# Optimization experiments

Hardware: AMD Instinct MI355X
Metric: run time of the kernel (lower is better)

Reference implementation:

```python
import jax, jax.numpy as jnp
import numpy as np

B, T_CTX, N_EMBD, N_ATTN, N_HEAD = 8, 1024, 1024, 1024, 16
HEAD_SIZE = N_ATTN // N_HEAD


def _init_time_w():
    # replicates the torch init: per-head exponential decay curves
    curve = np.array([-(T_CTX - 1 - i) for i in range(T_CTX)], dtype=np.float64)
    ww = np.ones((N_HEAD, T_CTX), dtype=np.float32)
    for h in range(N_HEAD):
        if h < N_HEAD - 1:
            decay_speed = T_CTX ** (-(h + 1) / (N_HEAD - 1))
        else:
            decay_speed = 0.0
        ww[h] = np.exp(curve * decay_speed).astype(np.float32)
    return jnp.asarray(ww)


def setup_inputs() -> dict:
    key = jax.random.key(0)
    ks = jax.random.split(key, 6)
    s = 0.02
    return {
        "x": jax.random.normal(ks[0], (B, T_CTX, N_EMBD), jnp.float32),
        "time_w": _init_time_w(),                                   # [H, TT]
        "time_alpha": jnp.ones((N_HEAD, 1, T_CTX), jnp.float32),
        "time_beta": jnp.ones((N_HEAD, T_CTX, 1), jnp.float32),
        "time_gamma": jnp.ones((T_CTX, 1), jnp.float32),
        "Wk": jax.random.normal(ks[1], (N_ATTN, N_EMBD), jnp.float32) * s,
        "bk": jnp.zeros((N_ATTN,), jnp.float32),
        "Wv": jax.random.normal(ks[2], (N_ATTN, N_EMBD), jnp.float32) * s,
        "bv": jnp.zeros((N_ATTN,), jnp.float32),
        "Wr": jax.random.normal(ks[3], (N_ATTN, N_EMBD), jnp.float32) * s,
        "br": jnp.zeros((N_ATTN,), jnp.float32),
        "Wo": jax.random.normal(ks[4], (N_EMBD, N_ATTN), jnp.float32) * s,
        "bo": jnp.zeros((N_EMBD,), jnp.float32),
    }


def _build_w(time_w, time_alpha, time_beta, T):
    # w[h,t,u] = time_w[h, TT-1-(t-u)] for u<=t else 0  (causal decay matrix)
    TT = time_w.shape[1]
    t = jnp.arange(T)[:, None]
    u = jnp.arange(T)[None, :]
    idx = jnp.clip((TT - 1) - t + u, 0, TT - 1)
    mask = u <= t
    w = jnp.where(mask[None, :, :], time_w[:, idx], 0.0)  # [H, T, T]
    return w * time_alpha[:, :, :T] * time_beta[:, :T, :]


def reference(x, time_w, time_alpha, time_beta, time_gamma,
              Wk, bk, Wv, bv, Wr, br, Wo, bo):
    Bb, T, C = x.shape
    H = time_w.shape[0]
    w = _build_w(time_w, time_alpha, time_beta, T)  # [H,T,T]

    # time shift on the first half of channels: prepend zero row, drop last
    x_half = jnp.pad(x[:, :, : C // 2], ((0, 0), (1, 0), (0, 0)))[:, :T, :]
    xs = jnp.concatenate([x_half, x[:, :, C // 2 :]], axis=-1)

    k = xs @ Wk.T + bk
    v = xs @ Wv.T + bv
    r = xs @ Wr.T + br

    k = jnp.exp(jnp.clip(k, -60.0, 30.0))
    sum_k = jnp.cumsum(k, axis=1)  # [B,T,NA]

    kv = (k * v).reshape(Bb, T, H, -1)               # [B,T,H,hs]
    wkv = jnp.einsum('htu,buhc->bthc', w, kv).reshape(Bb, T, -1)

    rwkv = jax.nn.sigmoid(r) * wkv / sum_k
    out = rwkv @ Wo.T + bo
    return out * time_gamma[:T]
```

## Files before the change

kernel.cpp:

```cpp
#include <hip/hip_runtime.h>
#include <hip/hip_bf16.h>
#include <cstddef>
#include <cstdint>

#define B_SZ   8
#define T_CTX  1024
#define C_DIM  1024
#define H_NUM  16
#define HS     64
#define M_ROWS (B_SZ * T_CTX)

typedef __attribute__((ext_vector_type(8))) short bf16x8;
typedef __attribute__((ext_vector_type(8))) unsigned short u16x8;
typedef __attribute__((ext_vector_type(4))) float f32x4;

static __device__ inline unsigned short f2bf(float f) {
    __hip_bfloat16 h = __float2bfloat16(f);
    return __builtin_bit_cast(unsigned short, h);
}
static __device__ inline float bf2f(unsigned short u) {
    unsigned int v = ((unsigned int)u) << 16;
    return __builtin_bit_cast(float, v);
}
static __device__ inline void gld16(const void* g, void* l) {
    __builtin_amdgcn_global_load_lds((const __attribute__((address_space(1))) void*)g,
                                     (__attribute__((address_space(3))) void*)l,
                                     16, 0, 0);
}

__global__ __launch_bounds__(256)
void convert_all(const float* __restrict__ x, unsigned short* __restrict__ xs,
                 const float* __restrict__ Wk, const float* __restrict__ Wv,
                 const float* __restrict__ Wr, const float* __restrict__ Wo,
                 unsigned short* __restrict__ wdst)
{
    const int bid = blockIdx.x;
    if (bid < 8192) {
        const int idx = (bid * 256 + threadIdx.x) * 4;
        const int m = idx >> 10;
        const int c = idx & 1023;
        float4 v;
        if (c < 512) {
            const int t = m & (T_CTX - 1);
            if (t == 0) v = make_float4(0.f, 0.f, 0.f, 0.f);
            else        v = *(const float4*)(x + (size_t)(m - 1) * C_DIM + c);
        } else {
            v = *(const float4*)(x + idx);
        }
        ushort4 o;
        o.x = f2bf(v.x); o.y = f2bf(v.y); o.z = f2bf(v.z); o.w = f2bf(v.w);
        *(ushort4*)(xs + idx) = o;
    } else {
        const int wid = bid - 8192;
        const int z = wid >> 10;
        const float* src = (z == 0) ? Wk : (z == 1) ? Wv : (z == 2) ? Wr : Wo;
        const int idx = ((wid & 1023) * 256 + threadIdx.x) * 4;
        const float4 v = *(const float4*)(src + idx);
        ushort4 o;
        o.x = f2bf(v.x); o.y = f2bf(v.y); o.z = f2bf(v.z); o.w = f2bf(v.w);
        *(ushort4*)(wdst + (size_t)z * (C_DIM * C_DIM) + idx) = o;
    }
}

__global__ __launch_bounds__(256, 2)
void mfma_gemm64(const unsigned short* __restrict__ A,
                 const unsigned short* __restrict__ Wb,
                 const float* __restrict__ b0, const float* __restrict__ b1,
                 const float* __restrict__ b2,
                 void* __restrict__ o0, void* __restrict__ o1, void* __restrict__ o2,
                 const float* __restrict__ gamma, int multi)
{
    const int d  = blockIdx.x;
    const int y  = ((d & 7) << 3) | ((d >> 3) & 7);
    const int xb = d >> 6;
    const int m0 = y * 128, n0 = xb * 128;

    int mode, ncol0;
    const float* bias;
    void* out;
    if (multi) {
        const int z = n0 >> 10;
        mode = z;
        ncol0 = n0 & 1023;
        bias = (z == 0) ? b0 : (z == 1) ? b1 : b2;
        out  = (z == 0) ? o0 : (z == 1) ? o1 : o2;
    } else {
        mode = 3; ncol0 = n0; bias = b0; out = o0;
    }

    __shared__ unsigned short As[128 * 64];
    __shared__ unsigned short Bs[128 * 64];

    const int tid = threadIdx.x;
    const int w = tid >> 6, l = tid & 63;

    const int r8  = l >> 3;
    const int c16 = ((l & 7) ^ r8) * 8;
    const unsigned short* gA = A  + (size_t)(m0 + w * 32 + r8) * C_DIM + c16;
    const unsigned short* gB = Wb + (size_t)(n0 + w * 32 + r8) * C_DIM + c16;
    char* lA = (char*)As + (w * 32) * 128;
    char* lB = (char*)Bs + (w * 32) * 128;

    const int wr = w >> 1, wc = w & 1;
    const int lr = l & 15, lkq = l >> 4;
    const int x7 = lr & 7;

    f32x4 acc[4][4];
    #pragma unroll
    for (int i = 0; i < 4; ++i)
        #pragma unroll
        for (int j = 0; j < 4; ++j) acc[i][j] = (f32x4){0.f, 0.f, 0.f, 0.f};

    for (int k0 = 0; k0 < C_DIM; k0 += 64) {
        #pragma unroll
        for (int r = 0; r < 4; ++r) {
            gld16(gA + k0 + (size_t)r * 8 * C_DIM, lA + r * 8 * 128);
            gld16(gB + k0 + (size_t)r * 8 * C_DIM, lB + r * 8 * 128);
        }
        __syncthreads();

        bf16x8 af[2][4], bfv[2][4];
        #pragma unroll
        for (int ks = 0; ks < 2; ++ks) {
            const int slot = ((ks * 4 + lkq) ^ x7) * 8;
            #pragma unroll
            for (int i = 0; i < 4; ++i)
                af[ks][i] = *(const bf16x8*)&As[(wr * 64 + i * 16 + lr) * 64 + slot];
            #pragma unroll
            for (int j = 0; j < 4; ++j)
                bfv[ks][j] = *(const bf16x8*)&Bs[(wc * 64 + j * 16 + lr) * 64 + slot];
        }
        #pragma unroll
        for (int ks = 0; ks < 2; ++ks)
            #pragma unroll
            for (int i = 0; i < 4; ++i)
                #pragma unroll
                for (int j = 0; j < 4; ++j)
                    acc[i][j] = __builtin_amdgcn_mfma_f32_16x16x32_bf16(
                        af[ks][i], bfv[ks][j], acc[i][j], 0, 0, 0);
        __syncthreads();
    }

    #pragma unroll
    for (int j = 0; j < 4; ++j) {
        const int col = ncol0 + wc * 64 + j * 16 + lr;
        const float bz = bias[col];
        #pragma unroll
        for (int i = 0; i < 4; ++i) {
            const int rb = m0 + wr * 64 + i * 16 + lkq * 4;
            #pragma unroll
            for (int r = 0; r < 4; ++r) {
                const int row = rb + r;
                float v = acc[i][j][r] + bz;
                if (mode == 0)      v = __expf(fminf(fmaxf(v, -60.f), 30.f));
                else if (mode == 2) v = 1.f / (1.f + __expf(-v));
                else if (mode == 3) v *= gamma[row & (T_CTX - 1)];
                if (mode == 1 || mode == 2)
                    ((unsigned short*)out)[(size_t)row * C_DIM + col] = f2bf(v);
                else
                    ((float*)out)[(size_t)row * C_DIM + col] = v;
            }
        }
    }
}

__global__ __launch_bounds__(256)
void cumsum_chunk(const float* __restrict__ expk, const unsigned short* __restrict__ vbf,
                  const float* __restrict__ alpha,
                  float* __restrict__ sumk, unsigned short* __restrict__ kvT,
                  float* __restrict__ aux)
{
    const int n = blockIdx.x * 256 + threadIdx.x;
    const int q = blockIdx.y;
    const int b = blockIdx.z;
    const int h = n >> 6, c = n & 63;
    const size_t base = ((size_t)b * T_CTX + q * 64) * C_DIM + n;
    unsigned short* kvrow = kvT + (((size_t)b * H_NUM + h) * HS + c) * T_CTX + q * 64;
    const float* arow = alpha + h * T_CTX + q * 64;
    float s = 0.f;
    for (int g = 0; g < 8; ++g) {
        u16x8 buf;
        #pragma unroll
        for (int k = 0; k < 8; ++k) {
            const int i = g * 8 + k;
            const size_t idx = base + (size_t)i * C_DIM;
            const float e  = expk[idx];
            const float vv = bf2f(vbf[idx]);
            s += e;
            sumk[idx] = s;
            buf[k] = f2bf(e * vv * arow[i]);
        }
        *(u16x8*)(kvrow + g * 8) = buf;
    }
    aux[((size_t)b * 16 + q) * C_DIM + n] = s;
}

#define REPL_STRIDE 1176
#define REPL_USED   1168

__global__ __launch_bounds__(256)
void wkv_mfma(const unsigned short* __restrict__ kvT,
              const float* __restrict__ sumk,
              const unsigned short* __restrict__ sigr,
              const float* __restrict__ tw, const float* __restrict__ beta,
              const float* __restrict__ aux,
              unsigned short* __restrict__ rwkv)
{
    __shared__ unsigned short repl[8 * REPL_STRIDE];
    __shared__ unsigned short kv_s[64 * 72];
    __shared__ unsigned short tw_s[1024];

    const int tid = threadIdx.x;
    const int bx = blockIdx.x;
    const int t0 = bx * 128;
    const int h  = blockIdx.y;
    const int b  = blockIdx.z;

    {
        const int i = tid * 4;
        const float4 v = *(const float4*)(tw + h * T_CTX + i);
        ushort4 o;
        o.x = f2bf(v.x); o.y = f2bf(v.y); o.z = f2bf(v.z); o.w = f2bf(v.w);
        *(ushort4*)&tw_s[i] = o;
    }
    __syncthreads();

    #pragma unroll
    for (int r = 0; r < 8; ++r)
        for (int i = tid; i < REPL_USED; i += 256) {
            const int src = i + r;
            repl[r * REPL_STRIDE + i] = (src < 1024) ? tw_s[src] : (unsigned short)0;
        }
    __syncthreads();

    const int w = tid >> 6, l = tid & 63;
    const int wr = w >> 1, wc = w & 1;
    const int lr = l & 15, lkq = l >> 4;

    const int r    = (7 - lr) & 7;
    const int S0   = 1023 - t0 - wr * 64 - lr + lkq * 8;
    const int abase = 2 * S0 + (2 * REPL_STRIDE - 2) * r;
    const char* repl_c = (const char*)repl;

    const int srow = tid >> 2;
    const int ucol = (tid & 3) * 16;
    const unsigned short* gkv = kvT + (((size_t)b * H_NUM + h) * HS + srow) * T_CTX + ucol;
    unsigned short* skv = &kv_s[srow * 72 + ucol];

    f32x4 acc[4][2];
    #pragma unroll
    for (int i = 0; i < 4; ++i) {
        acc[i][0] = (f32x4){0.f, 0.f, 0.f, 0.f};
        acc[i][1] = (f32x4){0.f, 0.f, 0.f, 0.f};
    }

    const int nsteps = t0 / 64 + 2;
    u16x8 q0 = *(const u16x8*)(gkv);
    u16x8 q1 = *(const u16x8*)(gkv + 8);
    for (int ks = 0; ks < nsteps; ++ks) {
        __syncthreads();
        *(u16x8*)skv       = q0;
        *(u16x8*)(skv + 8) = q1;
        __syncthreads();
        if (ks + 1 < nsteps) {
            const int un = (ks + 1) * 64;
            q0 = *(const u16x8*)(gkv + un);
            q1 = *(const u16x8*)(gkv + un + 8);
        }

        const int ub = abase + 2 * (ks * 64);
        #pragma unroll
        for (int kk = 0; kk < 2; ++kk) {
            bf16x8 af[4], bfv[2];
            #pragma unroll
            for (int i = 0; i < 4; ++i)
                af[i] = *(const bf16x8*)(repl_c + (ub + kk * 64 - i * 32));
            #pragma unroll
            for (int j = 0; j < 2; ++j)
                bfv[j] = *(const bf16x8*)&kv_s[(wc * 32 + j * 16 + lr) * 72 + kk * 32 + lkq * 8];
            #pragma unroll
            for (int i = 0; i < 4; ++i)
                #pragma unroll
                for (int j = 0; j < 2; ++j)
                    acc[i][j] = __builtin_amdgcn_mfma_f32_16x16x32_bf16(
                        af[i], bfv[j], acc[i][j], 0, 0, 0);
        }
    }

    const int cq = 2 * bx + wr;
    float off[2];
    #pragma unroll
    for (int j = 0; j < 2; ++j) {
        const int cl = wc * 32 + j * 16 + lr;
        float o = 0.f;
        for (int q = 0; q < cq; ++q)
            o += aux[((size_t)b * 16 + q) * C_DIM + h * HS + cl];
        off[j] = o;
    }

    #pragma unroll
    for (int i = 0; i < 4; ++i) {
        const int tb = t0 + wr * 64 + i * 16 + lkq * 4;
        #pragma unroll
        for (int rg = 0; rg < 4; ++rg) {
            const int t = tb + rg;
            const float bet = beta[h * T_CTX + t];
            const size_t row_off = ((size_t)(b * T_CTX + t)) * C_DIM + h * HS;
            #pragma unroll
            for (int j = 0; j < 2; ++j) {
                const int cl = wc * 32 + j * 16 + lr;
                const float sk = sumk[row_off + cl] + off[j];
                const float sr = bf2f(sigr[row_off + cl]);
                rwkv[row_off + cl] = f2bf(sr * bet * acc[i][j][rg] / sk);
            }
        }
    }
}

extern "C" void kernel_launch(void* const* d_in, const int* in_sizes, int n_in,
                              void* d_out, int out_size, void* d_ws, size_t ws_size,
                              hipStream_t stream)
{
    const float* x     = (const float*)d_in[0];
    const float* tw    = (const float*)d_in[1];
    const float* alpha = (const float*)d_in[2];
    const float* beta  = (const float*)d_in[3];
    const float* gamma = (const float*)d_in[4];
    const float* Wk    = (const float*)d_in[5];
    const float* bk    = (const float*)d_in[6];
    const float* Wv    = (const float*)d_in[7];
    const float* bv    = (const float*)d_in[8];
    const float* Wr    = (const float*)d_in[9];
    const float* br    = (const float*)d_in[10];
    const float* Wo    = (const float*)d_in[11];
    const float* bo    = (const float*)d_in[12];
    float* out = (float*)d_out;

    char* W = (char*)d_ws;
    float* expk          = (float*)W;
    unsigned short* rwkv = (unsigned short*)W;
    unsigned short* vbf  = (unsigned short*)(W + (32ull << 20));
    unsigned short* wbf  = (unsigned short*)(W + (48ull << 20));
    float* aux           = (float*)(W + (56ull << 20));
    float* sumk          = (float*)(W + (64ull << 20));
    unsigned short* xs   = (unsigned short*)(W + (64ull << 20));
    unsigned short* sigr = (unsigned short*)(W + (96ull << 20));
    unsigned short* kvT  = (unsigned short*)(W + (112ull << 20));

    const size_t WSZ = (size_t)C_DIM * C_DIM;

    convert_all<<<dim3(12288), 256, 0, stream>>>(x, xs, Wk, Wv, Wr, Wo, wbf);

    mfma_gemm64<<<dim3(1536), 256, 0, stream>>>(
        xs, wbf, bk, bv, br, expk, vbf, sigr, gamma, 1);

    cumsum_chunk<<<dim3(4, 16, 8), 256, 0, stream>>>(expk, vbf, alpha, sumk, kvT, aux);

    wkv_mfma<<<dim3(8, 16, 8), 256, 0, stream>>>(
        kvT, sumk, sigr, tw, beta, aux, rwkv);

    mfma_gemm64<<<dim3(512), 256, 0, stream>>>(
        rwkv, wbf + 3 * WSZ, bo, nullptr, nullptr,
        out, nullptr, nullptr, gamma, 0);
}
```

Measured before the change: 277.2 us.

## Add 8-wave triple-buffered 128x256 GEMM for fused K/V/R projection

Replaces the 128x128 fused K/V/R projection GEMM with a new 512-thread kernel that computes 128x256 tiles. It triple-buffers the shared-memory stages and interleaves global prefetch with MFMA phases using explicit waitcnt, barriers and setprio. The larger tile reuses each loaded A tile across more columns, and the pipeline aims to hide load latency. In exchange it runs one block per CU with heavy LDS use (144KB), and the grid is remapped for L2 locality. The output GEMM is simplified to a single-mode kernel.

```diff
diff --git a/kernel.cpp b/kernel.cpp
--- a/kernel.cpp
+++ b/kernel.cpp
@@ -62,31 +62,192 @@
     }
 }
 
+__global__ __launch_bounds__(512, 1)
+void mfma_gemm8p(const unsigned short* __restrict__ A,
+                 const unsigned short* __restrict__ Wb,
+                 const float* __restrict__ b0, const float* __restrict__ b1,
+                 const float* __restrict__ b2,
+                 void* __restrict__ o0, void* __restrict__ o1, void* __restrict__ o2)
+{
+    const int dblk = blockIdx.x;
+    const int g = (dblk & 7) * 96 + (dblk >> 3);
+    const int ty = g / 12, tx = g - ty * 12;
+    const int m0 = ty * 128, n0 = tx * 256;
+    const int z = n0 >> 10;
+    const int ncol0 = n0 & 1023;
+    const float* bias = (z == 0) ? b0 : (z == 1) ? b1 : b2;
+    void* out = (z == 0) ? o0 : (z == 1) ? o1 : o2;
+
+    __shared__ unsigned short As[3 * 8192];
+    __shared__ unsigned short Bs[3 * 16384];
+    char* const As_c = (char*)As;
+    char* const Bs_c = (char*)Bs;
+
+    const int tid = threadIdx.x;
+    const int w = tid >> 6, l = tid & 63;
+
+    const int trow = tid >> 3;
+    const int tchk = (tid & 7) ^ (trow & 7);
+    const unsigned short* gA0 = A  + (size_t)(m0 + trow) * C_DIM + tchk * 8;
+    const unsigned short* gB0 = Wb + (size_t)(n0 + trow) * C_DIM + tchk * 8;
+    const int woff = w * 1024;
+
+    auto stA = [&](int kt, int h, int ds) {
+        gld16(gA0 + (size_t)h * 64 * C_DIM + kt * 64,
+              As_c + ds * 16384 + h * 8192 + woff);
+    };
+    auto stB = [&](int kt, int h, int ds) {
+        const unsigned short* p = gB0 + (size_t)h * 128 * C_DIM + kt * 64;
+        char* q = Bs_c + ds * 32768 + h * 16384 + woff;
+        gld16(p, q);
+        gld16(p + (size_t)64 * C_DIM, q + 8192);
+    };
+
+    const int wr = w >> 2, wc = w & 3;
+    const int lr = l & 15, lkq = l >> 4;
+    const int x7 = lr & 7;
+    const int ks0b = ((lkq)     ^ x7) * 16;
+    const int ks1b = ((4 + lkq) ^ x7) * 16;
+    const int abase = wr * 8192 + lr * 128;
+    const int bbase = (wc >> 1) * 16384 + ((wc & 1) * 64 + lr) * 128;
+
+    bf16x8 af0, af1, bfr[4];
+    f32x4 acc[4][4];
+    #pragma unroll
+    for (int i = 0; i < 4; ++i)
+        #pragma unroll
+        for (int j = 0; j < 4; ++j) acc[i][j] = (f32x4){0.f, 0.f, 0.f, 0.f};
+
+    stA(0, 0, 0); stA(0, 1, 0); stB(0, 0, 0); stB(0, 1, 0);
+    stA(1, 0, 1); stA(1, 1, 1); stB(1, 0, 1); stB(1, 1, 1);
+    asm volatile("s_waitcnt vmcnt(6)" ::: "memory");
+    __builtin_amdgcn_s_barrier();
+    __builtin_amdgcn_sched_barrier(0);
+
+    int d = 0, d2 = 2;
+    for (int kt = 0; kt < 16; ++kt) {
+        const char* Ad = As_c + d * 16384 + abase;
+        const char* Bd = Bs_c + d * 32768 + bbase;
+
+        af0 = *(const bf16x8*)(Ad + 0 * 2048 + ks0b);
+        af1 = *(const bf16x8*)(Ad + 1 * 2048 + ks0b);
+        bfr[0] = *(const bf16x8*)(Bd + 0 * 2048 + ks0b);
+        bfr[1] = *(const bf16x8*)(Bd + 1 * 2048 + ks0b);
+        bfr[2] = *(const bf16x8*)(Bd + 2 * 2048 + ks0b);
+        bfr[3] = *(const bf16x8*)(Bd + 3 * 2048 + ks0b);
+        if (kt < 14) stA(kt + 2, 0, d2);
+        __builtin_amdgcn_sched_barrier(0);
+        __builtin_amdgcn_s_barrier();
+        asm volatile("s_waitcnt lgkmcnt(0)" ::: "memory");
+        __builtin_amdgcn_sched_barrier(0);
+        __builtin_amdgcn_s_setprio(1);
+        #pragma unroll
+        for (int j = 0; j < 4; ++j) {
+            acc[0][j] = __builtin_amdgcn_mfma_f32_16x16x32_bf16(af0, bfr[j], acc[0][j], 0, 0, 0);
+            acc[1][j] = __builtin_amdgcn_mfma_f32_16x16x32_bf16(af1, bfr[j], acc[1][j], 0, 0, 0);
+        }
+        __builtin_amdgcn_s_setprio(0);
+        __builtin_amdgcn_sched_barrier(0);
+        __builtin_amdgcn_s_barrier();
+
+        af0 = *(const bf16x8*)(Ad + 2 * 2048 + ks0b);
+        af1 = *(const bf16x8*)(Ad + 3 * 2048 + ks0b);
+        if (kt < 14) stA(kt + 2, 1, d2);
+        __builtin_amdgcn_sched_barrier(0);
+        __builtin_amdgcn_s_barrier();
+        asm volatile("s_waitcnt lgkmcnt(0)" ::: "memory");
+        __builtin_amdgcn_sched_barrier(0);
+        __builtin_amdgcn_s_setprio(1);
+        #pragma unroll
+        for (int j = 0; j < 4; ++j) {
+            acc[2][j] = __builtin_amdgcn_mfma_f32_16x16x32_bf16(af0, bfr[j], acc[2][j], 0, 0, 0);
+            acc[3][j] = __builtin_amdgcn_mfma_f32_16x16x32_bf16(af1, bfr[j], acc[3][j], 0, 0, 0);
+        }
+        __builtin_amdgcn_s_setprio(0);
+        __builtin_amdgcn_sched_barrier(0);
+        __builtin_amdgcn_s_barrier();
+
+        af0 = *(const bf16x8*)(Ad + 0 * 2048 + ks1b);
+        af1 = *(const bf16x8*)(Ad + 1 * 2048 + ks1b);
+        bfr[0] = *(const bf16x8*)(Bd + 0 * 2048 + ks1b);
+        bfr[1] = *(const bf16x8*)(Bd + 1 * 2048 + ks1b);
+        bfr[2] = *(const bf16x8*)(Bd + 2 * 2048 + ks1b);
+        bfr[3] = *(const bf16x8*)(Bd + 3 * 2048 + ks1b);
+        if (kt < 14) stB(kt + 2, 0, d2);
+        __builtin_amdgcn_sched_barrier(0);
+        __builtin_amdgcn_s_barrier();
+        asm volatile("s_waitcnt lgkmcnt(0)" ::: "memory");
+        __builtin_amdgcn_sched_barrier(0);
+        __builtin_amdgcn_s_setprio(1);
+        #pragma unroll
+        for (int j = 0; j < 4; ++j) {
+            acc[0][j] = __builtin_amdgcn_mfma_f32_16x16x32_bf16(af0, bfr[j], acc[0][j], 0, 0, 0);
+            acc[1][j] = __builtin_amdgcn_mfma_f32_16x16x32_bf16(af1, bfr[j], acc[1][j], 0, 0, 0);
+        }
+        __builtin_amdgcn_s_setprio(0);
+        __builtin_amdgcn_sched_barrier(0);
+        __builtin_amdgcn_s_barrier();
+
+        af0 = *(const bf16x8*)(Ad + 2 * 2048 + ks1b);
+        af1 = *(const bf16x8*)(Ad + 3 * 2048 + ks1b);
+        if (kt < 14) stB(kt + 2, 1, d2);
+        if (kt < 14)       asm volatile("s_waitcnt vmcnt(6)" ::: "memory");
+        else if (kt == 14) asm volatile("s_waitcnt vmcnt(0)" ::: "memory");
+        __builtin_amdgcn_sched_barrier(0);
+        __builtin_amdgcn_s_barrier();
+        asm volatile("s_waitcnt lgkmcnt(0)" ::: "memory");
+        __builtin_amdgcn_sched_barrier(0);
+        __builtin_amdgcn_s_setprio(1);
+        #pragma unroll
+        for (int j = 0; j < 4; ++j) {
+            acc[2][j] = __builtin_amdgcn_mfma_f32_16x16x32_bf16(af0, bfr[j], acc[2][j], 0, 0, 0);
+            acc[3][j] = __builtin_amdgcn_mfma_f32_16x16x32_bf16(af1, bfr[j], acc[3][j], 0, 0, 0);
+        }
+        __builtin_amdgcn_s_setprio(0);
+        __builtin_amdgcn_sched_barrier(0);
+        __builtin_amdgcn_s_barrier();
+
+        const int dn = (d == 2) ? 0 : d + 1;
+        d2 = d;
+        d = dn;
+    }
+
+    #pragma unroll
+    for (int j = 0; j < 4; ++j) {
+        const int col = ncol0 + wc * 64 + j * 16 + lr;
+        const float bz = bias[col];
+        #pragma unroll
+        for (int i = 0; i < 4; ++i) {
+            const int rb = m0 + wr * 64 + i * 16 + lkq * 4;
+            #pragma unroll
+            for (int r = 0; r < 4; ++r) {
+                const int row = rb + r;
+                float v = acc[i][j][r] + bz;
+                if (z == 0) {
+                    v = __expf(fminf(fmaxf(v, -60.f), 30.f));
+                    ((float*)out)[(size_t)row * C_DIM + col] = v;
+                } else if (z == 2) {
+                    v = 1.f / (1.f + __expf(-v));
+                    ((unsigned short*)out)[(size_t)row * C_DIM + col] = f2bf(v);
+                } else {
+                    ((unsigned short*)out)[(size_t)row * C_DIM + col] = f2bf(v);
+                }
+            }
+        }
+    }
+}
+
 __global__ __launch_bounds__(256, 2)
 void mfma_gemm64(const unsigned short* __restrict__ A,
                  const unsigned short* __restrict__ Wb,
-                 const float* __restrict__ b0, const float* __restrict__ b1,
-                 const float* __restrict__ b2,
-                 void* __restrict__ o0, void* __restrict__ o1, void* __restrict__ o2,
-                 const float* __restrict__ gamma, int multi)
+                 const float* __restrict__ b0,
+                 void* __restrict__ o0,
+                 const float* __restrict__ gamma)
 {
     const int d  = blockIdx.x;
     const int y  = ((d & 7) << 3) | ((d >> 3) & 7);
     const int xb = d >> 6;
     const int m0 = y * 128, n0 = xb * 128;
-
-    int mode, ncol0;
-    const float* bias;
-    void* out;
-    if (multi) {
-        const int z = n0 >> 10;
-        mode = z;
-        ncol0 = n0 & 1023;
-        bias = (z == 0) ? b0 : (z == 1) ? b1 : b2;
-        out  = (z == 0) ? o0 : (z == 1) ? o1 : o2;
-    } else {
-        mode = 3; ncol0 = n0; bias = b0; out = o0;
-    }
 
     __shared__ unsigned short As[128 * 64];
     __shared__ unsigned short Bs[128 * 64];
@@ -143,22 +304,16 @@
 
     #pragma unroll
     for (int j = 0; j < 4; ++j) {
-        const int col = ncol0 + wc * 64 + j * 16 + lr;
-        const float bz = bias[col];
+        const int col = n0 + wc * 64 + j * 16 + lr;
+        const float bz = b0[col];
         #pragma unroll
         for (int i = 0; i < 4; ++i) {
             const int rb = m0 + wr * 64 + i * 16 + lkq * 4;
             #pragma unroll
             for (int r = 0; r < 4; ++r) {
                 const int row = rb + r;
-                float v = acc[i][j][r] + bz;
-                if (mode == 0)      v = __expf(fminf(fmaxf(v, -60.f), 30.f));
-                else if (mode == 2) v = 1.f / (1.f + __expf(-v));
-                else if (mode == 3) v *= gamma[row & (T_CTX - 1)];
-                if (mode == 1 || mode == 2)
-                    ((unsigned short*)out)[(size_t)row * C_DIM + col] = f2bf(v);
-                else
-                    ((float*)out)[(size_t)row * C_DIM + col] = v;
+                float v = (acc[i][j][r] + bz) * gamma[row & (T_CTX - 1)];
+                ((float*)o0)[(size_t)row * C_DIM + col] = v;
             }
         }
     }
@@ -351,8 +506,8 @@
 
     convert_all<<<dim3(12288), 256, 0, stream>>>(x, xs, Wk, Wv, Wr, Wo, wbf);
 
-    mfma_gemm64<<<dim3(1536), 256, 0, stream>>>(
-        xs, wbf, bk, bv, br, expk, vbf, sigr, gamma, 1);
+    mfma_gemm8p<<<dim3(768), 512, 0, stream>>>(
+        xs, wbf, bk, bv, br, expk, vbf, sigr);
 
     cumsum_chunk<<<dim3(4, 16, 8), 256, 0, stream>>>(expk, vbf, alpha, sumk, kvT, aux);
 
@@ -360,6 +515,5 @@
         kvT, sumk, sigr, tw, beta, aux, rwkv);
 
     mfma_gemm64<<<dim3(512), 256, 0, stream>>>(
-        rwkv, wbf + 3 * WSZ, bo, nullptr, nullptr,
-        out, nullptr, nullptr, gamma, 0);
-}
+        rwkv, wbf + 3 * WSZ, bo, out, gamma);
+}
```

Result: slower. 285.5 us (+3.0%).
